# Performance work log

Hardware: AMD Instinct MI355X
Metric: run time of the kernel (lower is better)

The kernel has to match this reference:

```python
import jax, jax.numpy as jnp
import numpy as np

B, S, HID = 2, 2048, 2048
NH, NKV, DH = 16, 4, 128
EPS = 1e-6

def rotate_half(x):
    x1, x2 = x[..., : x.shape[-1] // 2], x[..., x.shape[-1] // 2 :]
    return jnp.concatenate((-x2, x1), axis=-1)

def rms_norm(x, w):
    var = jnp.mean(jnp.square(x), axis=-1, keepdims=True)
    return w * (x * jax.lax.rsqrt(var + EPS))

def setup_inputs() -> dict:
    key = jax.random.key(0)
    ks = jax.random.split(key, 8)
    hidden_states = jax.random.normal(ks[0], (B, S, HID), dtype=jnp.float32)
    # causal additive mask, broadcastable to [B, H, S, S]
    causal = jnp.tril(jnp.ones((S, S), dtype=bool))
    attention_mask = jnp.where(causal, 0.0, -1e9).astype(jnp.float32)[None, None]
    # RoPE tables: [1, S, 1, DH] to broadcast over (B, S, H, DH)
    inv_freq = 1.0 / (10000.0 ** (np.arange(0, DH, 2, dtype=np.float32) / DH))
    t = np.arange(S, dtype=np.float32)
    freqs = np.einsum('s,d->sd', t, inv_freq)
    emb = np.concatenate([freqs, freqs], axis=-1)  # [S, DH]
    cos = jnp.asarray(np.cos(emb))[None, :, None, :]
    sin = jnp.asarray(np.sin(emb))[None, :, None, :]
    std = 0.02
    Wq = jax.random.normal(ks[1], (HID, NH * DH), dtype=jnp.float32) * std
    Wk = jax.random.normal(ks[2], (HID, NKV * DH), dtype=jnp.float32) * std
    Wv = jax.random.normal(ks[3], (HID, NKV * DH), dtype=jnp.float32) * std
    Wo = jax.random.normal(ks[4], (NH * DH, HID), dtype=jnp.float32) * std
    q_norm_w = jnp.ones((DH,), dtype=jnp.float32)
    k_norm_w = jnp.ones((DH,), dtype=jnp.float32)
    return dict(hidden_states=hidden_states, attention_mask=attention_mask,
                cos=cos, sin=sin, Wq=Wq, Wk=Wk, Wv=Wv, Wo=Wo,
                q_norm_w=q_norm_w, k_norm_w=k_norm_w)

def reference(hidden_states, attention_mask, cos, sin, Wq, Wk, Wv, Wo, q_norm_w, k_norm_w):
    b, s, _ = hidden_states.shape
    q = (hidden_states @ Wq).reshape(b, s, NH, DH)
    k = (hidden_states @ Wk).reshape(b, s, NKV, DH)
    v = (hidden_states @ Wv).reshape(b, s, NKV, DH)
    # per-head RMSNorm on q/k
    q = rms_norm(q, q_norm_w)
    k = rms_norm(k, k_norm_w)
    # RoPE
    q = q * cos + rotate_half(q) * sin
    k = k * cos + rotate_half(k) * sin
    # GQA: repeat kv heads
    groups = NH // NKV
    k = jnp.repeat(k, groups, axis=2)
    v = jnp.repeat(v, groups, axis=2)
    scale = 1.0 / jnp.sqrt(jnp.asarray(DH, dtype=q.dtype))
    scores = jnp.einsum('bqhd,bkhd->bhqk', q, k) * scale  # [B,H,S,S]
    scores = scores + attention_mask
    probs = jax.nn.softmax(scores, axis=-1)
    out = jnp.einsum('bhqk,bkhd->bqhd', probs, v)
    out = out.reshape(b, s, NH * DH)
    return out @ Wo
```

## Files before the change

### kernel.cpp

```cpp
#include <hip/hip_runtime.h>
#include <hip/hip_bf16.h>
#include <stdint.h>


typedef __attribute__((ext_vector_type(8))) short short8;
typedef __attribute__((ext_vector_type(4))) float floatx4;
typedef __hip_bfloat16 bf16_t;

#define MFMA16x16(a, b, c) __builtin_amdgcn_mfma_f32_16x16x32_bf16(a, b, c, 0, 0, 0)

__device__ __forceinline__ void async_copy16(const void* g, void* l) {
  __builtin_amdgcn_global_load_lds(
      (const __attribute__((address_space(1))) void*)g,
      (__attribute__((address_space(3))) void*)l, 16, 0, 0);
}

__device__ __forceinline__ unsigned short bf16bits(float x) {
  bf16_t h = __float2bfloat16(x);
  return *reinterpret_cast<unsigned short*>(&h);
}

__global__ __launch_bounds__(256) void convbf_kernel(const float* __restrict__ in,
                                                     bf16_t* __restrict__ out, int n4) {
  int i = blockIdx.x * 256 + threadIdx.x;
  if (i < n4) {
    const float4 v = reinterpret_cast<const float4*>(in)[i];
    ushort4 o;
    o.x = bf16bits(v.x); o.y = bf16bits(v.y); o.z = bf16bits(v.z); o.w = bf16bits(v.w);
    reinterpret_cast<ushort4*>(out)[i] = o;
  }
}

__global__ __launch_bounds__(256) void wtrans_kernel(const float* __restrict__ W,
                                                     bf16_t* __restrict__ Wt, int N, int roff) {
  __shared__ float t[32][33];
  int k0 = blockIdx.y * 32, n0 = blockIdx.x * 32;
#pragma unroll
  for (int j = 0; j < 4; ++j)
    t[threadIdx.y + j * 8][threadIdx.x] =
        W[(size_t)(k0 + threadIdx.y + j * 8) * N + n0 + threadIdx.x];
  __syncthreads();
#pragma unroll
  for (int j = 0; j < 4; ++j) {
    int n = n0 + threadIdx.y + j * 8, k = k0 + threadIdx.x;
    Wt[(size_t)(roff + n) * 2048 + k] = __float2bfloat16(t[threadIdx.x][threadIdx.y + j * 8]);
  }
}

template <int OBF>
__global__ __launch_bounds__(256, 3) void gemm_bt_kernel(const bf16_t* __restrict__ A,
                                                         const bf16_t* __restrict__ Bt,
                                                         void* __restrict__ Cv,
                                                         int K, int ldc) {
  __shared__ __align__(16) char smem[32768];
  const int tid = threadIdx.x;
  const int wave = tid >> 6, lane = tid & 63;
  const int wr = wave >> 1, wc = wave & 1;
  const int l16 = lane & 15, lhi = lane >> 4;

  const int nwg = gridDim.x * gridDim.y;
  const int orig = blockIdx.y * gridDim.x + blockIdx.x;
  const int swz = (orig & 7) * (nwg >> 3) + (orig >> 3);
  const int bn = (swz % gridDim.x) * 128;
  const int bm = (swz / gridDim.x) * 128;

  floatx4 acc[4][4] = {};

  for (int k0 = 0; k0 < K; k0 += 64) {
    __syncthreads();
#pragma unroll
    for (int i = 0; i < 4; ++i) {
      int chunk = i * 4 + wave;
      unsigned p = (unsigned)chunk * 1024u + (unsigned)lane * 16u;
      unsigned row = p >> 7;
      unsigned colg = (p & 127u) ^ ((row & 7u) << 4);
      const char* gA = (const char*)(A + (size_t)(bm + row) * K + k0) + colg;
      async_copy16(gA, smem + (size_t)chunk * 1024);
      const char* gB = (const char*)(Bt + (size_t)(bn + row) * K + k0) + colg;
      async_copy16(gB, smem + 16384 + (size_t)chunk * 1024);
    }
    __syncthreads();
#pragma unroll
    for (int kk = 0; kk < 2; ++kk) {
      short8 fa[4], fb[4];
#pragma unroll
      for (int mi = 0; mi < 4; ++mi) {
        unsigned row = wr * 64 + mi * 16 + l16;
        unsigned off = row * 128u + kk * 64u + lhi * 16u;
        off ^= (row & 7u) << 4;
        fa[mi] = *(const short8*)(smem + off);
      }
#pragma unroll
      for (int ni = 0; ni < 4; ++ni) {
        unsigned row = wc * 64 + ni * 16 + l16;
        unsigned off = row * 128u + kk * 64u + lhi * 16u;
        off ^= (row & 7u) << 4;
        fb[ni] = *(const short8*)(smem + 16384 + off);
      }
#pragma unroll
      for (int mi = 0; mi < 4; ++mi)
#pragma unroll
        for (int ni = 0; ni < 4; ++ni)
          acc[mi][ni] = MFMA16x16(fa[mi], fb[ni], acc[mi][ni]);
    }
  }
#pragma unroll
  for (int mi = 0; mi < 4; ++mi)
#pragma unroll
    for (int ni = 0; ni < 4; ++ni)
#pragma unroll
      for (int r = 0; r < 4; ++r) {
        int row = bm + wr * 64 + mi * 16 + lhi * 4 + r;
        int col = bn + wc * 64 + ni * 16 + l16;
        if (OBF)
          ((bf16_t*)Cv)[(size_t)row * ldc + col] = __float2bfloat16(acc[mi][ni][r]);
        else
          ((float*)Cv)[(size_t)row * ldc + col] = acc[mi][ni][r];
      }
}

__global__ __launch_bounds__(256) void qknorm_rope_kernel(
    const bf16_t* __restrict__ Cqkv, const float* __restrict__ cosT,
    const float* __restrict__ sinT, const float* __restrict__ qw,
    const float* __restrict__ kw, bf16_t* __restrict__ Qa, bf16_t* __restrict__ Ka) {
  int wave = threadIdx.x >> 6, lane = threadIdx.x & 63;
  int task = blockIdx.x * 4 + wave;
  int unit = task % 20;
  int row = task / 20;
  int b = row >> 11, s = row & 2047;
  const bf16_t* src;
  const float* w;
  bf16_t* dst;
  float sc;
  if (unit < 16) {
    src = Cqkv + (size_t)row * 3072 + unit * 128;
    w = qw;
    dst = Qa + ((size_t)(b * 16 + unit) * 2048 + s) * 128;
    sc = 0.088388347648318447f;
  } else {
    int kh = unit - 16;
    src = Cqkv + (size_t)row * 3072 + 2048 + kh * 128;
    w = kw;
    dst = Ka + ((size_t)(b * 4 + kh) * 2048 + s) * 128;
    sc = 1.0f;
  }
  float x1 = __bfloat162float(src[lane]), x2 = __bfloat162float(src[lane + 64]);
  float ss = x1 * x1 + x2 * x2;
#pragma unroll
  for (int off = 1; off < 64; off <<= 1) ss += __shfl_xor(ss, off, 64);
  float inv = rsqrtf(ss * (1.f / 128.f) + 1e-6f);
  x1 = x1 * inv * w[lane];
  x2 = x2 * inv * w[lane + 64];
  float c1 = cosT[(size_t)s * 128 + lane], c2 = cosT[(size_t)s * 128 + lane + 64];
  float s1 = sinT[(size_t)s * 128 + lane], s2 = sinT[(size_t)s * 128 + lane + 64];
  dst[lane] = __float2bfloat16((x1 * c1 - x2 * s1) * sc);
  dst[lane + 64] = __float2bfloat16((x2 * c2 + x1 * s2) * sc);
}

__global__ __launch_bounds__(256) void vtrans_kernel(const bf16_t* __restrict__ Cqkv,
                                                     bf16_t* __restrict__ Vt) {
  __shared__ bf16_t t[32][33];
  int bk = blockIdx.z;
  int b = bk >> 2, kh = bk & 3;
  int s0 = blockIdx.x * 32, d0 = blockIdx.y * 32;
  const bf16_t* src = Cqkv + (size_t)(b * 2048) * 3072 + 2560 + kh * 128;
#pragma unroll
  for (int j = 0; j < 4; ++j)
    t[threadIdx.y + j * 8][threadIdx.x] =
        src[(size_t)(s0 + threadIdx.y + j * 8) * 3072 + d0 + threadIdx.x];
  __syncthreads();
  bf16_t* dst = Vt + (size_t)(b * 4 + kh) * 128 * 2048;
#pragma unroll
  for (int j = 0; j < 4; ++j) {
    int d = d0 + threadIdx.y + j * 8, s = s0 + threadIdx.x;
    dst[(size_t)d * 2048 + s] = t[threadIdx.x][threadIdx.y + j * 8];
  }
}

__device__ __forceinline__ unsigned swz_row(unsigned row) {
  return (((row & 7u) ^ ((row >> 3) << 1)) & 7u) << 4;
}

__global__ __launch_bounds__(256, 2) void flash_kernel(const bf16_t* __restrict__ Qa,
                                                       const bf16_t* __restrict__ Ka,
                                                       const bf16_t* __restrict__ Vt,
                                                       bf16_t* __restrict__ attnO) {
  __shared__ __align__(16) char smem[32768];
  const int tid = threadIdx.x;
  const int wave = tid >> 6, lane = tid & 63;
  const int l16 = lane & 15, lhi = lane >> 4;
  const int bid = blockIdx.x;
  const int bh = bid & 31;
  const int ib = bid >> 5;
  const int qb = (ib < 8) ? (15 - ib) : (ib - 8);
  const int h = bh & 15, b = bh >> 4;
  const int kh = h >> 2;
  const int q0b = qb << 7;
  const int q0w = q0b + wave * 32;

  const bf16_t* Qb = Qa + ((size_t)bh * 2048 + q0w) * 128;
  const bf16_t* Kb = Ka + (size_t)(b * 4 + kh) * 2048 * 128;
  const bf16_t* Vb = Vt + (size_t)(b * 4 + kh) * 128 * 2048;

  char* Kl = smem;
  char* Vl = smem + 16384;

  short8 qf[2][4];
#pragma unroll
  for (int rt = 0; rt < 2; ++rt)
#pragma unroll
    for (int kk = 0; kk < 4; ++kk)
      qf[rt][kk] = *(const short8*)(Qb + (size_t)(rt * 16 + l16) * 128 + kk * 32 + lhi * 8);

  short8 onesf;
#pragma unroll
  for (int j = 0; j < 8; ++j) onesf[j] = (short)0x3F80;

  floatx4 o[2][8] = {};
  floatx4 lsum[2] = {};
  short8 pf[2][2];
  float m[2] = {-1e30f, -1e30f};

  const float THR = 8.0f;
  const int nch = 2 * qb + 2;

#pragma unroll
  for (int it = 0; it < 4; ++it) {
    unsigned p = (unsigned)(it * 4 + wave) * 1024u + (unsigned)lane * 16u;
    unsigned row = p >> 8;
    unsigned gcol = (p & 255u) ^ swz_row(row);
    async_copy16((const char*)(Kb + (size_t)row * 128) + gcol,
                 smem + (size_t)(it * 4 + wave) * 1024);
  }
#pragma unroll
  for (int it = 0; it < 4; ++it) {
    unsigned p = (unsigned)(it * 4 + wave) * 1024u + (unsigned)lane * 16u;
    unsigned row = p >> 7;
    unsigned gcol = (p & 127u) ^ swz_row(row);
    async_copy16((const char*)(Vb + (size_t)row * 2048) + gcol,
                 Vl + (size_t)(it * 4 + wave) * 1024);
  }
  __syncthreads();

  for (int c = 0; c < nch; ++c) {
    const int kc0 = c << 6;
    const bool active = (kc0 <= q0w + 31);

    if (active) {
      floatx4 s[2][4] = {};
      __builtin_amdgcn_s_setprio(1);
#pragma unroll
      for (int g = 0; g < 4; ++g) {
        unsigned row = (unsigned)(l16 >> 2) * 8u + (unsigned)((g & 1) * 4) +
                       (unsigned)(l16 & 3) + (unsigned)((g >> 1) * 32);
        unsigned base = row * 256u;
        unsigned px = swz_row(row);
#pragma unroll
        for (int kk = 0; kk < 4; ++kk) {
          short8 kf = *(const short8*)(Kl + base + (((unsigned)(kk * 64 + lhi * 16)) ^ px));
          s[0][g] = MFMA16x16(kf, qf[0][kk], s[0][g]);
          s[1][g] = MFMA16x16(kf, qf[1][kk], s[1][g]);
        }
      }
      __builtin_amdgcn_s_setprio(0);

      const bool needMask = (kc0 + 64 > q0w);
#pragma unroll
      for (int rt = 0; rt < 2; ++rt) {
        const int qrow = q0w + rt * 16 + l16;
        if (needMask) {
#pragma unroll
          for (int g = 0; g < 4; ++g)
#pragma unroll
            for (int r = 0; r < 4; ++r) {
              int key = kc0 + lhi * 8 + (g & 1) * 4 + r + (g >> 1) * 32;
              if (key > qrow) s[rt][g][r] = -1e9f;
            }
        }
        float mx = s[rt][0][0];
#pragma unroll
        for (int g = 0; g < 4; ++g)
#pragma unroll
          for (int r = 0; r < 4; ++r) mx = fmaxf(mx, s[rt][g][r]);
        mx = fmaxf(mx, __shfl_xor(mx, 16, 64));
        mx = fmaxf(mx, __shfl_xor(mx, 32, 64));
        bool grow = mx > m[rt] + THR;
        if (__any(grow)) {
          float mn = fmaxf(m[rt], mx);
          float corr = __expf(m[rt] - mn);
          m[rt] = mn;
#pragma unroll
          for (int r = 0; r < 4; ++r) {
            float co = __shfl(corr, lhi * 4 + r, 64);
            lsum[rt][r] *= co;
#pragma unroll
            for (int f = 0; f < 8; ++f) o[rt][f][r] *= co;
          }
        }
#pragma unroll
        for (int ks = 0; ks < 2; ++ks) {
          union { unsigned u[4]; short8 v; } pk;
#pragma unroll
          for (int half = 0; half < 2; ++half) {
            int g = ks * 2 + half;
            float p0 = __expf(s[rt][g][0] - m[rt]);
            float p1 = __expf(s[rt][g][1] - m[rt]);
            float p2 = __expf(s[rt][g][2] - m[rt]);
            float p3 = __expf(s[rt][g][3] - m[rt]);
            pk.u[half * 2] = (unsigned)bf16bits(p0) | ((unsigned)bf16bits(p1) << 16);
            pk.u[half * 2 + 1] = (unsigned)bf16bits(p2) | ((unsigned)bf16bits(p3) << 16);
          }
          pf[rt][ks] = pk.v;
        }
      }
    }

    __syncthreads();

    if (c + 1 < nch) {
#pragma unroll
      for (int it = 0; it < 4; ++it) {
        unsigned p = (unsigned)(it * 4 + wave) * 1024u + (unsigned)lane * 16u;
        unsigned row = p >> 8;
        unsigned gcol = (p & 255u) ^ swz_row(row);
        async_copy16((const char*)(Kb + (size_t)(kc0 + 64 + row) * 128) + gcol,
                     Kl + (size_t)(it * 4 + wave) * 1024);
      }
    }

    if (active) {
      __builtin_amdgcn_s_setprio(1);
#pragma unroll
      for (int ks = 0; ks < 2; ++ks) {
#pragma unroll
        for (int f = 0; f < 8; ++f) {
          unsigned row = (unsigned)(f * 16 + l16);
          short8 vf = *(const short8*)(Vl + row * 128u +
                                       (((unsigned)(ks * 64 + lhi * 16)) ^ swz_row(row)));
          o[0][f] = MFMA16x16(pf[0][ks], vf, o[0][f]);
          o[1][f] = MFMA16x16(pf[1][ks], vf, o[1][f]);
        }
        lsum[0] = MFMA16x16(pf[0][ks], onesf, lsum[0]);
        lsum[1] = MFMA16x16(pf[1][ks], onesf, lsum[1]);
      }
      __builtin_amdgcn_s_setprio(0);
    }

    __syncthreads();

    if (c + 1 < nch) {
#pragma unroll
      for (int it = 0; it < 4; ++it) {
        unsigned p = (unsigned)(it * 4 + wave) * 1024u + (unsigned)lane * 16u;
        unsigned row = p >> 7;
        unsigned gcol = (p & 127u) ^ swz_row(row);
        async_copy16((const char*)(Vb + (size_t)row * 2048 + kc0 + 64) + gcol,
                     Vl + (size_t)(it * 4 + wave) * 1024);
      }
    }
  }

#pragma unroll
  for (int rt = 0; rt < 2; ++rt)
#pragma unroll
    for (int r = 0; r < 4; ++r) {
      float inv = 1.f / lsum[rt][r];
      int row = q0w + rt * 16 + lhi * 4 + r;
      size_t base = ((size_t)(b * 2048) + row) * 2048 + h * 128;
#pragma unroll
      for (int f = 0; f < 8; ++f)
        attnO[base + f * 16 + l16] = __float2bfloat16(o[rt][f][r] * inv);
    }
}

extern "C" void kernel_launch(void* const* d_in, const int* in_sizes, int n_in,
                              void* d_out, int out_size, void* d_ws, size_t ws_size,
                              hipStream_t stream) {
  const float* hs = (const float*)d_in[0];
  const float* cosT = (const float*)d_in[2];
  const float* sinT = (const float*)d_in[3];
  const float* Wq = (const float*)d_in[4];
  const float* Wk = (const float*)d_in[5];
  const float* Wv = (const float*)d_in[6];
  const float* Wo = (const float*)d_in[7];
  const float* qw = (const float*)d_in[8];
  const float* kw = (const float*)d_in[9];
  float* out = (float*)d_out;

  char* ws = (char*)d_ws;
  size_t off = 0;
  auto alloc = [&](size_t bytes) {
    char* p = ws + off;
    off += (bytes + 255) & ~(size_t)255;
    return p;
  };
  bf16_t* hsb  = (bf16_t*)alloc((size_t)4096 * 2048 * 2);
  bf16_t* wqkv = (bf16_t*)alloc((size_t)3072 * 2048 * 2);
  bf16_t* wot  = (bf16_t*)alloc((size_t)2048 * 2048 * 2);
  bf16_t* cqkv = (bf16_t*)alloc((size_t)4096 * 3072 * 2);
  bf16_t* qa   = (bf16_t*)alloc((size_t)2 * 16 * 2048 * 128 * 2);
  bf16_t* ka   = (bf16_t*)alloc((size_t)2 * 4 * 2048 * 128 * 2);
  bf16_t* vt   = (bf16_t*)alloc((size_t)2 * 4 * 2048 * 128 * 2);
  bf16_t* attn = (bf16_t*)cqkv;

  convbf_kernel<<<8192, 256, 0, stream>>>(hs, hsb, 2097152);
  dim3 tb(32, 8);
  wtrans_kernel<<<dim3(64, 64), tb, 0, stream>>>(Wq, wqkv, 2048, 0);
  wtrans_kernel<<<dim3(16, 64), tb, 0, stream>>>(Wk, wqkv, 512, 2048);
  wtrans_kernel<<<dim3(16, 64), tb, 0, stream>>>(Wv, wqkv, 512, 2560);
  wtrans_kernel<<<dim3(64, 64), tb, 0, stream>>>(Wo, wot, 2048, 0);
  gemm_bt_kernel<1><<<dim3(24, 32), 256, 0, stream>>>(hsb, wqkv, cqkv, 2048, 3072);
  qknorm_rope_kernel<<<20480, 256, 0, stream>>>(cqkv, cosT, sinT, qw, kw, qa, ka);
  vtrans_kernel<<<dim3(64, 4, 8), tb, 0, stream>>>(cqkv, vt);
  flash_kernel<<<512, 256, 0, stream>>>(qa, ka, vt, attn);
  gemm_bt_kernel<0><<<dim3(16, 32), 256, 0, stream>>>(attn, wot, out, 2048, 2048);
}
```

Measured before the change: 196.5 us.

## Double-buffer K/V tiles in flash attention with async prefetch of next chunk

Doubles the LDS allocation to 64 KB so the next K and V chunk is loaded asynchronously into a second buffer while the current one is computed. Two full __syncthreads per iteration become explicit vmcnt waits plus raw barriers, and QK^T, softmax and PV run without an intervening barrier. This is meant to hide global-to-LDS load latency. The cost is higher LDS use per block, which may reduce occupancy from the two blocks per CU the launch bounds request. The hand-written waitcnt counts also add correctness risk.

```diff
diff --git a/kernel.cpp b/kernel.cpp
--- a/kernel.cpp
+++ b/kernel.cpp
@@ -185,7 +185,7 @@
                                                        const bf16_t* __restrict__ Ka,
                                                        const bf16_t* __restrict__ Vt,
                                                        bf16_t* __restrict__ attnO) {
-  __shared__ __align__(16) char smem[32768];
+  __shared__ __align__(16) char smem[65536];
   const int tid = threadIdx.x;
   const int wave = tid >> 6, lane = tid & 63;
   const int l16 = lane & 15, lhi = lane >> 4;
@@ -202,9 +202,6 @@
   const bf16_t* Kb = Ka + (size_t)(b * 4 + kh) * 2048 * 128;
   const bf16_t* Vb = Vt + (size_t)(b * 4 + kh) * 128 * 2048;
 
-  char* Kl = smem;
-  char* Vl = smem + 16384;
-
   short8 qf[2][4];
 #pragma unroll
   for (int rt = 0; rt < 2; ++rt)
@@ -224,27 +221,47 @@
   const float THR = 8.0f;
   const int nch = 2 * qb + 2;
 
-#pragma unroll
-  for (int it = 0; it < 4; ++it) {
-    unsigned p = (unsigned)(it * 4 + wave) * 1024u + (unsigned)lane * 16u;
-    unsigned row = p >> 8;
-    unsigned gcol = (p & 255u) ^ swz_row(row);
-    async_copy16((const char*)(Kb + (size_t)row * 128) + gcol,
-                 smem + (size_t)(it * 4 + wave) * 1024);
-  }
-#pragma unroll
-  for (int it = 0; it < 4; ++it) {
-    unsigned p = (unsigned)(it * 4 + wave) * 1024u + (unsigned)lane * 16u;
-    unsigned row = p >> 7;
-    unsigned gcol = (p & 127u) ^ swz_row(row);
-    async_copy16((const char*)(Vb + (size_t)row * 2048) + gcol,
-                 Vl + (size_t)(it * 4 + wave) * 1024);
-  }
-  __syncthreads();
-
+  auto stageK = [&](int key0, char* dstK) {
+#pragma unroll
+    for (int it = 0; it < 4; ++it) {
+      unsigned p = (unsigned)(it * 4 + wave) * 1024u + (unsigned)lane * 16u;
+      unsigned row = p >> 8;
+      unsigned gcol = (p & 255u) ^ swz_row(row);
+      async_copy16((const char*)(Kb + (size_t)(key0 + row) * 128) + gcol,
+                   dstK + (size_t)(it * 4 + wave) * 1024);
+    }
+  };
+  auto stageV = [&](int key0, char* dstV) {
+#pragma unroll
+    for (int it = 0; it < 4; ++it) {
+      unsigned p = (unsigned)(it * 4 + wave) * 1024u + (unsigned)lane * 16u;
+      unsigned row = p >> 7;
+      unsigned gcol = (p & 127u) ^ swz_row(row);
+      async_copy16((const char*)(Vb + (size_t)row * 2048 + key0) + gcol,
+                   dstV + (size_t)(it * 4 + wave) * 1024);
+    }
+  };
+
+  stageK(0, smem);
+  stageV(0, smem + 16384);
+
+  int cur = 0;
   for (int c = 0; c < nch; ++c) {
     const int kc0 = c << 6;
     const bool active = (kc0 <= q0w + 31);
+    char* Kl = smem + (size_t)cur * 32768;
+    char* Vl = Kl + 16384;
+    char* Kn = smem + (size_t)(cur ^ 1) * 32768;
+
+    if (c + 1 < nch) {
+      stageK(kc0 + 64, Kn);
+      stageV(kc0 + 64, Kn + 16384);
+      asm volatile("s_waitcnt vmcnt(8)" ::: "memory");
+    } else {
+      asm volatile("s_waitcnt vmcnt(0)" ::: "memory");
+    }
+    __builtin_amdgcn_s_barrier();
+    __builtin_amdgcn_sched_barrier(0);
 
     if (active) {
       floatx4 s[2][4] = {};
@@ -313,22 +330,7 @@
           pf[rt][ks] = pk.v;
         }
       }
-    }
-
-    __syncthreads();
-
-    if (c + 1 < nch) {
-#pragma unroll
-      for (int it = 0; it < 4; ++it) {
-        unsigned p = (unsigned)(it * 4 + wave) * 1024u + (unsigned)lane * 16u;
-        unsigned row = p >> 8;
-        unsigned gcol = (p & 255u) ^ swz_row(row);
-        async_copy16((const char*)(Kb + (size_t)(kc0 + 64 + row) * 128) + gcol,
-                     Kl + (size_t)(it * 4 + wave) * 1024);
-      }
-    }
-
-    if (active) {
+
       __builtin_amdgcn_s_setprio(1);
 #pragma unroll
       for (int ks = 0; ks < 2; ++ks) {
@@ -346,18 +348,8 @@
       __builtin_amdgcn_s_setprio(0);
     }
 
-    __syncthreads();
-
-    if (c + 1 < nch) {
-#pragma unroll
-      for (int it = 0; it < 4; ++it) {
-        unsigned p = (unsigned)(it * 4 + wave) * 1024u + (unsigned)lane * 16u;
-        unsigned row = p >> 7;
-        unsigned gcol = (p & 127u) ^ swz_row(row);
-        async_copy16((const char*)(Vb + (size_t)row * 2048 + kc0 + 64) + gcol,
-                     Vl + (size_t)(it * 4 + wave) * 1024);
-      }
-    }
+    __builtin_amdgcn_s_barrier();
+    cur ^= 1;
   }
 
 #pragma unroll
```

Result: slower. 203.1 us (+3.3%).

## Split KV range for long causal query blocks and merge partials

Applied to the files above, without the earlier changes.

Query blocks in the upper half of the sequence now process their causal key range in two independent halves, each writing unnormalized bf16 partial outputs plus row max and sum. A new combine kernel rescales and merges the two halves into the attention output. This balances per-block work and raises the block count (with occupancy bound raised to 3) to cut the tail imbalance of causal attention. It adds an extra launch, partial-buffer traffic reusing dead workspace, and bf16 rounding of partials.

```diff
diff --git a/kernel.cpp b/kernel.cpp
--- a/kernel.cpp
+++ b/kernel.cpp
@@ -181,18 +181,29 @@
   return (((row & 7u) ^ ((row >> 3) << 1)) & 7u) << 4;
 }
 
-__global__ __launch_bounds__(256, 2) void flash_kernel(const bf16_t* __restrict__ Qa,
+__global__ __launch_bounds__(256, 3) void flash_kernel(const bf16_t* __restrict__ Qa,
                                                        const bf16_t* __restrict__ Ka,
                                                        const bf16_t* __restrict__ Vt,
-                                                       bf16_t* __restrict__ attnO) {
+                                                       bf16_t* __restrict__ attnO,
+                                                       bf16_t* __restrict__ Opart,
+                                                       float* __restrict__ Ml) {
   __shared__ __align__(16) char smem[32768];
   const int tid = threadIdx.x;
   const int wave = tid >> 6, lane = tid & 63;
   const int l16 = lane & 15, lhi = lane >> 4;
   const int bid = blockIdx.x;
   const int bh = bid & 31;
-  const int ib = bid >> 5;
-  const int qb = (ib < 8) ? (15 - ib) : (ib - 8);
+  const int task = bid >> 5;
+  int qb, cBeg, cEnd, halfB = 0;
+  bool split;
+  if (task < 8) {
+    qb = task; split = false; cBeg = 0; cEnd = 2 * qb + 2;
+  } else {
+    int idx = task - 8;
+    qb = 8 + (idx >> 1); halfB = idx & 1; split = true;
+    if (!halfB) { cBeg = 0; cEnd = qb + 1; }
+    else        { cBeg = qb + 1; cEnd = 2 * qb + 2; }
+  }
   const int h = bh & 15, b = bh >> 4;
   const int kh = h >> 2;
   const int q0b = qb << 7;
@@ -222,27 +233,33 @@
   float m[2] = {-1e30f, -1e30f};
 
   const float THR = 8.0f;
-  const int nch = 2 * qb + 2;
-
-#pragma unroll
-  for (int it = 0; it < 4; ++it) {
-    unsigned p = (unsigned)(it * 4 + wave) * 1024u + (unsigned)lane * 16u;
-    unsigned row = p >> 8;
-    unsigned gcol = (p & 255u) ^ swz_row(row);
-    async_copy16((const char*)(Kb + (size_t)row * 128) + gcol,
-                 smem + (size_t)(it * 4 + wave) * 1024);
-  }
-#pragma unroll
-  for (int it = 0; it < 4; ++it) {
-    unsigned p = (unsigned)(it * 4 + wave) * 1024u + (unsigned)lane * 16u;
-    unsigned row = p >> 7;
-    unsigned gcol = (p & 127u) ^ swz_row(row);
-    async_copy16((const char*)(Vb + (size_t)row * 2048) + gcol,
-                 Vl + (size_t)(it * 4 + wave) * 1024);
-  }
+
+  auto stageK = [&](int key0) {
+#pragma unroll
+    for (int it = 0; it < 4; ++it) {
+      unsigned p = (unsigned)(it * 4 + wave) * 1024u + (unsigned)lane * 16u;
+      unsigned row = p >> 8;
+      unsigned gcol = (p & 255u) ^ swz_row(row);
+      async_copy16((const char*)(Kb + (size_t)(key0 + row) * 128) + gcol,
+                   Kl + (size_t)(it * 4 + wave) * 1024);
+    }
+  };
+  auto stageV = [&](int key0) {
+#pragma unroll
+    for (int it = 0; it < 4; ++it) {
+      unsigned p = (unsigned)(it * 4 + wave) * 1024u + (unsigned)lane * 16u;
+      unsigned row = p >> 7;
+      unsigned gcol = (p & 127u) ^ swz_row(row);
+      async_copy16((const char*)(Vb + (size_t)row * 2048 + key0) + gcol,
+                   Vl + (size_t)(it * 4 + wave) * 1024);
+    }
+  };
+
+  stageK(cBeg << 6);
+  stageV(cBeg << 6);
   __syncthreads();
 
-  for (int c = 0; c < nch; ++c) {
+  for (int c = cBeg; c < cEnd; ++c) {
     const int kc0 = c << 6;
     const bool active = (kc0 <= q0w + 31);
 
@@ -317,16 +334,7 @@
 
     __syncthreads();
 
-    if (c + 1 < nch) {
-#pragma unroll
-      for (int it = 0; it < 4; ++it) {
-        unsigned p = (unsigned)(it * 4 + wave) * 1024u + (unsigned)lane * 16u;
-        unsigned row = p >> 8;
-        unsigned gcol = (p & 255u) ^ swz_row(row);
-        async_copy16((const char*)(Kb + (size_t)(kc0 + 64 + row) * 128) + gcol,
-                     Kl + (size_t)(it * 4 + wave) * 1024);
-      }
-    }
+    if (c + 1 < cEnd) stageK((c + 1) << 6);
 
     if (active) {
       __builtin_amdgcn_s_setprio(1);
@@ -348,29 +356,73 @@
 
     __syncthreads();
 
-    if (c + 1 < nch) {
-#pragma unroll
-      for (int it = 0; it < 4; ++it) {
-        unsigned p = (unsigned)(it * 4 + wave) * 1024u + (unsigned)lane * 16u;
-        unsigned row = p >> 7;
-        unsigned gcol = (p & 127u) ^ swz_row(row);
-        async_copy16((const char*)(Vb + (size_t)row * 2048 + kc0 + 64) + gcol,
-                     Vl + (size_t)(it * 4 + wave) * 1024);
-      }
-    }
-  }
-
-#pragma unroll
-  for (int rt = 0; rt < 2; ++rt)
-#pragma unroll
-    for (int r = 0; r < 4; ++r) {
-      float inv = 1.f / lsum[rt][r];
-      int row = q0w + rt * 16 + lhi * 4 + r;
-      size_t base = ((size_t)(b * 2048) + row) * 2048 + h * 128;
-#pragma unroll
-      for (int f = 0; f < 8; ++f)
-        attnO[base + f * 16 + l16] = __float2bfloat16(o[rt][f][r] * inv);
-    }
+    if (c + 1 < cEnd) stageV((c + 1) << 6);
+  }
+
+  if (!split) {
+#pragma unroll
+    for (int rt = 0; rt < 2; ++rt)
+#pragma unroll
+      for (int r = 0; r < 4; ++r) {
+        float inv = 1.f / lsum[rt][r];
+        int row = q0w + rt * 16 + lhi * 4 + r;
+        size_t base = ((size_t)(b * 2048) + row) * 2048 + h * 128;
+#pragma unroll
+        for (int f = 0; f < 8; ++f)
+          attnO[base + f * 16 + l16] = __float2bfloat16(o[rt][f][r] * inv);
+      }
+  } else {
+    const int pidx = ((bh << 3) + (qb - 8)) * 2 + halfB;
+    bf16_t* Ob = Opart + (size_t)pidx * 16384;
+    float* mlm = Ml + (size_t)pidx * 256;
+#pragma unroll
+    for (int rt = 0; rt < 2; ++rt) {
+#pragma unroll
+      for (int r = 0; r < 4; ++r) {
+        int rowt = wave * 32 + rt * 16 + lhi * 4 + r;
+#pragma unroll
+        for (int f = 0; f < 8; ++f)
+          Ob[(size_t)rowt * 128 + f * 16 + l16] = __float2bfloat16(o[rt][f][r]);
+        if (l16 == 0) mlm[128 + wave * 32 + rt * 16 + lhi * 4 + r] = lsum[rt][r];
+      }
+      if (lhi == 0) mlm[wave * 32 + rt * 16 + l16] = m[rt];
+    }
+  }
+}
+
+__global__ __launch_bounds__(256) void combine_kernel(const bf16_t* __restrict__ Opart,
+                                                      const float* __restrict__ Ml,
+                                                      bf16_t* __restrict__ attnO) {
+  const int tile = blockIdx.x;
+  const int bh = tile >> 3, qi = tile & 7, qb = 8 + qi;
+  const int h = bh & 15, b = bh >> 4;
+  const int row = threadIdx.x >> 1, half = threadIdx.x & 1;
+  const int pA = tile * 2, pB = pA + 1;
+  float mA = Ml[(size_t)pA * 256 + row], lA = Ml[(size_t)pA * 256 + 128 + row];
+  float mB = Ml[(size_t)pB * 256 + row], lB = Ml[(size_t)pB * 256 + 128 + row];
+  float M = fmaxf(mA, mB);
+  float wA = __expf(mA - M), wB = __expf(mB - M);
+  float inv = 1.f / (wA * lA + wB * lB);
+  const bf16_t* OA = Opart + (size_t)pA * 16384 + (size_t)row * 128 + half * 64;
+  const bf16_t* OB = Opart + (size_t)pB * 16384 + (size_t)row * 128 + half * 64;
+  size_t base = ((size_t)(b * 2048) + (qb << 7) + row) * 2048 + h * 128 + half * 64;
+#pragma unroll
+  for (int j = 0; j < 64; j += 8) {
+    short8 a8 = *(const short8*)(OA + j);
+    short8 b8 = *(const short8*)(OB + j);
+    ushort4 o0, o1;
+#pragma unroll
+    for (int e = 0; e < 8; ++e) {
+      unsigned short ua = (unsigned short)a8[e], ub = (unsigned short)b8[e];
+      float fa = __bfloat162float(*reinterpret_cast<bf16_t*>(&ua));
+      float fb = __bfloat162float(*reinterpret_cast<bf16_t*>(&ub));
+      unsigned short r = bf16bits((wA * fa + wB * fb) * inv);
+      if (e < 4) ((unsigned short*)&o0)[e] = r;
+      else       ((unsigned short*)&o1)[e - 4] = r;
+    }
+    *(ushort4*)(attnO + base + j) = o0;
+    *(ushort4*)(attnO + base + j + 4) = o1;
+  }
 }
 
 extern "C" void kernel_launch(void* const* d_in, const int* in_sizes, int n_in,
@@ -402,6 +454,8 @@
   bf16_t* ka   = (bf16_t*)alloc((size_t)2 * 4 * 2048 * 128 * 2);
   bf16_t* vt   = (bf16_t*)alloc((size_t)2 * 4 * 2048 * 128 * 2);
   bf16_t* attn = (bf16_t*)cqkv;
+  bf16_t* opart = (bf16_t*)hsb;
+  float*  mlbuf = (float*)wqkv;
 
   convbf_kernel<<<8192, 256, 0, stream>>>(hs, hsb, 2097152);
   dim3 tb(32, 8);
@@ -412,6 +466,7 @@
   gemm_bt_kernel<1><<<dim3(24, 32), 256, 0, stream>>>(hsb, wqkv, cqkv, 2048, 3072);
   qknorm_rope_kernel<<<20480, 256, 0, stream>>>(cqkv, cosT, sinT, qw, kw, qa, ka);
   vtrans_kernel<<<dim3(64, 4, 8), tb, 0, stream>>>(cqkv, vt);
-  flash_kernel<<<512, 256, 0, stream>>>(qa, ka, vt, attn);
+  flash_kernel<<<768, 256, 0, stream>>>(qa, ka, vt, attn, opart, mlbuf);
+  combine_kernel<<<256, 256, 0, stream>>>(opart, mlbuf, attn);
   gemm_bt_kernel<0><<<dim3(16, 32), 256, 0, stream>>>(attn, wot, out, 2048, 2048);
 }
```

New measurement: 251.1 us. +27.8%, slower.
